# Kernel optimization log

Measured on AMD Instinct MI355X. Metric: run time of the kernel, lower is better.

The kernel has to match this reference:

```python
import jax, jax.numpy as jnp
import numpy as np

EPS = 1e-6      # fast_transformers LinearAttention eps
LN_EPS = 1e-5   # torch LayerNorm default
L_LAYERS = 4
N_HEADS = 16
D_MODEL = 1024
D_FF = 4096


def _layernorm(x, g, b):
    mu = jnp.mean(x, axis=-1, keepdims=True)
    var = jnp.mean(jnp.square(x - mu), axis=-1, keepdims=True)
    return (x - mu) * jax.lax.rsqrt(var + LN_EPS) * g + b


def _layer(x, fmask, Wq, bq, Wk, bk, Wv, bv, Wo, bo, W1, b1, W2, b2, g1, be1, g2, be2):
    N, S, D = x.shape
    H = N_HEADS
    d = D // H
    q = (x @ Wq.T + bq).reshape(N, S, H, d)
    k = (x @ Wk.T + bk).reshape(N, S, H, d)
    v = (x @ Wv.T + bv).reshape(N, S, H, d)
    # feature map: elu(x) + 1
    Q = jax.nn.elu(q) + 1.0
    K = (jax.nn.elu(k) + 1.0) * fmask[:, :, None, None]
    # non-causal linear attention
    KV = jnp.einsum('nshd,nshm->nhmd', K, v)                       # [N,H,d,d]
    Z = 1.0 / (jnp.einsum('nlhd,nhd->nlh', Q, K.sum(axis=1)) + EPS)
    attn = jnp.einsum('nlhd,nhmd,nlh->nlhm', Q, KV, Z).reshape(N, S, D)
    x = x + (attn @ Wo.T + bo)
    y = x = _layernorm(x, g1, be1)
    y = jax.nn.gelu(y @ W1.T + b1, approximate=False) @ W2.T + b2
    return _layernorm(x + y, g2, be2)


def setup_inputs() -> dict:
    key = jax.random.key(0)
    ks = jax.random.split(key, 12)
    N, S, D, F = 4, 4096, D_MODEL, D_FF
    L = L_LAYERS
    s = 0.02
    inp = {
        'src': jax.random.normal(ks[0], (N, S, D), dtype=jnp.float32),
        'src_key_padding_mask': jnp.zeros((N, S), dtype=bool),
        'Wq': jax.random.normal(ks[1], (L, D, D), dtype=jnp.float32) * s,
        'bq': jnp.zeros((L, D), dtype=jnp.float32),
        'Wk': jax.random.normal(ks[2], (L, D, D), dtype=jnp.float32) * s,
        'bk': jnp.zeros((L, D), dtype=jnp.float32),
        'Wv': jax.random.normal(ks[3], (L, D, D), dtype=jnp.float32) * s,
        'bv': jnp.zeros((L, D), dtype=jnp.float32),
        'Wo': jax.random.normal(ks[4], (L, D, D), dtype=jnp.float32) * s,
        'bo': jnp.zeros((L, D), dtype=jnp.float32),
        'W1': jax.random.normal(ks[5], (L, F, D), dtype=jnp.float32) * s,
        'b1': jnp.zeros((L, F), dtype=jnp.float32),
        'W2': jax.random.normal(ks[6], (L, D, F), dtype=jnp.float32) * s,
        'b2': jnp.zeros((L, D), dtype=jnp.float32),
        'g1': jnp.ones((L, D), dtype=jnp.float32),
        'be1': jnp.zeros((L, D), dtype=jnp.float32),
        'g2': jnp.ones((L, D), dtype=jnp.float32),
        'be2': jnp.zeros((L, D), dtype=jnp.float32),
    }
    return inp


def reference(src, src_key_padding_mask, Wq, bq, Wk, bk, Wv, bv, Wo, bo,
              W1, b1, W2, b2, g1, be1, g2, be2):
    N, S, D = src.shape
    # LengthMask: valid positions are the first (S - num_paddings) tokens
    actual_len = S - src_key_padding_mask.sum(axis=1)              # [N]
    fmask = (jnp.arange(S)[None, :] < actual_len[:, None]).astype(src.dtype)
    x = src
    for i in range(L_LAYERS):
        x = _layer(x, fmask, Wq[i], bq[i], Wk[i], bk[i], Wv[i], bv[i],
                   Wo[i], bo[i], W1[i], b1[i], W2[i], b2[i],
                   g1[i], be1[i], g2[i], be2[i])
    return x
```

## Files before the change

kernel.cpp:

```cpp
#include <hip/hip_runtime.h>
#include <cstdint>

typedef unsigned short ushort_t;
typedef short v8s __attribute__((ext_vector_type(8)));
typedef float v4f __attribute__((ext_vector_type(4)));
typedef unsigned short v4u __attribute__((ext_vector_type(4)));

#define DMODEL 1024
#define DFF 4096
#define SEQ 4096
#define NBATCH 4
#define NHEAD 16
#define HDIM 64
#define NLAYER 4
#define MTOK (NBATCH*SEQ)

#define EPI_QKV 0
#define EPI_RES 3
#define EPI_GELU 4

__device__ __forceinline__ float bf2f(ushort_t u) {
    unsigned v = ((unsigned)u) << 16; float f; __builtin_memcpy(&f, &v, 4); return f;
}
__device__ __forceinline__ ushort_t f2bf(float f) {
    unsigned u; __builtin_memcpy(&u, &f, 4);
    u = (u + 0x7fffu + ((u >> 16) & 1u)) >> 16;
    return (ushort_t)u;
}

__device__ __forceinline__ float gelu_f(float x) {
    const float y = x * 0.70710678118f;
    const float ay = fabsf(y);
    const float t = __builtin_amdgcn_rcpf(1.f + 0.3275911f * ay);
    const float p = t * (0.254829592f + t * (-0.284496736f + t * (1.421413741f +
                    t * (-1.453152027f + t * 1.061405429f))));
    const float e = __expf(-y * y);
    float er = 1.f - p * e;
    er = (y < 0.f) ? -er : er;
    return 0.5f * x * (1.f + er);
}

__global__ __launch_bounds__(256) void cvt_bf16(const float* __restrict__ in,
                                                ushort_t* __restrict__ out, int n) {
    int i = (blockIdx.x * 256 + threadIdx.x) * 4;
    if (i >= n) return;
    float4 v = *(const float4*)(in + i);
    v4u o;
    o[0] = f2bf(v.x); o[1] = f2bf(v.y); o[2] = f2bf(v.z); o[3] = f2bf(v.w);
    *(v4u*)(out + i) = o;
}

__global__ __launch_bounds__(256) void cvt_qkv(const float* __restrict__ Wq,
                                               const float* __restrict__ Wk,
                                               const float* __restrict__ Wv,
                                               ushort_t* __restrict__ out) {
    const size_t DD = (size_t)DMODEL * DMODEL;
    size_t i = ((size_t)blockIdx.x * 256 + threadIdx.x) * 4;
    int l = (int)(i / DD);
    size_t r = i % DD;
    const float* srcs[3] = { Wq + l * DD + r, Wk + l * DD + r, Wv + l * DD + r };
    #pragma unroll
    for (int s = 0; s < 3; s++) {
        float4 v = *(const float4*)srcs[s];
        v4u o;
        o[0] = f2bf(v.x); o[1] = f2bf(v.y); o[2] = f2bf(v.z); o[3] = f2bf(v.w);
        *(v4u*)(out + ((size_t)l * 3 + s) * DD + r) = o;
    }
}

__global__ __launch_bounds__(256) void lens_kernel(const unsigned char* __restrict__ mask,
                                                   int* __restrict__ lens) {
    int lane = threadIdx.x & 63, w = threadIdx.x >> 6;
    int cnt = 0;
    for (int i = lane; i < SEQ; i += 64) cnt += (mask[w * SEQ + i] != 0) ? 1 : 0;
    #pragma unroll
    for (int off = 32; off; off >>= 1) cnt += __shfl_down(cnt, off);
    if (lane == 0) lens[w] = SEQ - cnt;
}

template <int EPI>
__global__ __launch_bounds__(256, 2) void gemm_bt(
    const ushort_t* __restrict__ A, const ushort_t* __restrict__ B,
    const float* __restrict__ bias, const float* __restrict__ bias2,
    const float* __restrict__ bias3, const float* res,
    const int* __restrict__ lens,
    ushort_t* __restrict__ outB, ushort_t* __restrict__ outB2,
    ushort_t* __restrict__ outB3, float* outF,
    int M, int N, int K)
{
    __shared__ __align__(16) ushort_t As[2][128 * 64];
    __shared__ __align__(16) ushort_t Bs[2][128 * 64];

    const int tid = threadIdx.x;
    const int lane = tid & 63;
    const int wave = tid >> 6;
    const int nb = N >> 7;
    const int xcd = blockIdx.x & 7;
    const int q = blockIdx.x >> 3;
    const int bm = (q / nb) * 8 + xcd;
    const int bn = q % nb;
    const int wm = (wave >> 1) * 64;
    const int wn = (wave & 1) * 64;
    const int lr = lane & 15;
    const int lq = lane >> 4;

    v4f acc[4][4];
    #pragma unroll
    for (int i = 0; i < 4; i++)
        #pragma unroll
        for (int j = 0; j < 4; j++) acc[i][j] = (v4f)0.f;

    const int srow = tid >> 3;
    const int schunk = (tid & 7) ^ (srow & 7);
    const ushort_t* Ag = A + (size_t)(bm * 128 + srow) * K + schunk * 8;
    const ushort_t* Bg = B + (size_t)(bn * 128 + srow) * K + schunk * 8;
    const size_t rstep = (size_t)32 * K;
    const int sdst = tid * 8;

    int a_off[2][4], b_off[2][4];
    #pragma unroll
    for (int h = 0; h < 2; h++)
        #pragma unroll
        for (int i = 0; i < 4; i++) {
            const int ra = wm + i * 16 + lr;
            a_off[h][i] = ra * 64 + (((h * 4 + lq) ^ (ra & 7)) * 8);
            const int rb = wn + i * 16 + lr;
            b_off[h][i] = rb * 64 + (((h * 4 + lq) ^ (rb & 7)) * 8);
        }

    v8s ra[4], rb[4];
    #pragma unroll
    for (int i = 0; i < 4; i++) ra[i] = *(const v8s*)(Ag + i * rstep);
    #pragma unroll
    for (int i = 0; i < 4; i++) rb[i] = *(const v8s*)(Bg + i * rstep);

    const int iters = K >> 6;
    int p = 0;
    for (int t = 0; t < iters; ++t) {
        #pragma unroll
        for (int i = 0; i < 4; i++) *(v8s*)&As[p][sdst + i * 2048] = ra[i];
        #pragma unroll
        for (int i = 0; i < 4; i++) *(v8s*)&Bs[p][sdst + i * 2048] = rb[i];
        if (t + 1 < iters) {
            const int k0 = (t + 1) << 6;
            #pragma unroll
            for (int i = 0; i < 4; i++) ra[i] = *(const v8s*)(Ag + i * rstep + k0);
            #pragma unroll
            for (int i = 0; i < 4; i++) rb[i] = *(const v8s*)(Bg + i * rstep + k0);
        }
        __syncthreads();
        #pragma unroll
        for (int h = 0; h < 2; h++) {
            v8s af[4], bfr[4];
            #pragma unroll
            for (int i = 0; i < 4; i++) af[i] = *(const v8s*)&As[p][a_off[h][i]];
            #pragma unroll
            for (int j = 0; j < 4; j++) bfr[j] = *(const v8s*)&Bs[p][b_off[h][j]];
            #pragma unroll
            for (int i = 0; i < 4; i++)
                #pragma unroll
                for (int j = 0; j < 4; j++)
                    acc[i][j] = __builtin_amdgcn_mfma_f32_16x16x32_bf16(af[i], bfr[j], acc[i][j], 0, 0, 0);
        }
        p ^= 1;
    }

    const int row0 = bm * 128 + wm + lq * 4;
    const int col0 = bn * 128 + wn + lr;

    const int seg = bn >> 3;
    ushort_t* qkv_out = (EPI == EPI_QKV)
        ? (seg == 0 ? outB : (seg == 1 ? outB2 : outB3)) : outB;
    const float* qkv_bias = (EPI == EPI_QKV)
        ? (seg == 0 ? bias : (seg == 1 ? bias2 : bias3)) : bias;
    const int blen = (EPI == EPI_QKV) ? lens[bm >> 5] : 0;

    #pragma unroll
    for (int i = 0; i < 4; i++) {
        #pragma unroll
        for (int j = 0; j < 4; j++) {
            const int gn = col0 + j * 16;
            const float bsv = (EPI == EPI_QKV) ? qkv_bias[gn & 1023] : bias[gn];
            #pragma unroll
            for (int r = 0; r < 4; r++) {
                const int gm = row0 + i * 16 + r;
                float v = acc[i][j][r] + bsv;
                if (EPI == EPI_QKV) {
                    const size_t oi = (size_t)gm * DMODEL + (gn & 1023);
                    if (seg == 2) {
                        qkv_out[oi] = f2bf(v);
                    } else {
                        float e = v > 0.f ? v + 1.f : __expf(v);
                        if (seg == 1 && (gm & 4095) >= blen) e = 0.f;
                        qkv_out[oi] = f2bf(e);
                    }
                } else if (EPI == EPI_RES) {
                    const size_t oi = (size_t)gm * N + gn;
                    outF[oi] = v + res[oi];
                } else {
                    const size_t oi = (size_t)gm * N + gn;
                    outB[oi] = f2bf(gelu_f(v));
                }
            }
        }
    }
}

__global__ __launch_bounds__(256) void ksum_kernel(const ushort_t* __restrict__ K,
                                                   float* __restrict__ out) {
    const int blk = blockIdx.x;
    const int n = blk >> 4, cg = blk & 15;
    const int tx = threadIdx.x & 63, ty = threadIdx.x >> 6;
    const int col = cg * 64 + tx;
    const ushort_t* p = K + ((size_t)n * SEQ + ty * 1024) * DMODEL + col;
    float a = 0.f;
    for (int s = 0; s < 1024; s++) a += bf2f(p[(size_t)s * DMODEL]);
    __shared__ float red[4][64];
    red[ty][tx] = a;
    __syncthreads();
    if (ty == 0) out[n * DMODEL + col] = red[0][tx] + red[1][tx] + red[2][tx] + red[3][tx];
}

__global__ __launch_bounds__(256) void kv_part(const ushort_t* __restrict__ K,
                                               const ushort_t* __restrict__ V,
                                               float* __restrict__ part) {
    const int chunk = blockIdx.x, nh = blockIdx.y;
    const int n = nh >> 4, h = nh & 15;
    const int tid = threadIdx.x;
    const int tm = tid >> 4, td = tid & 15;
    __shared__ float Ks[16][68];
    __shared__ float Vs[16][68];
    float acc[4][4] = {};
    const int s0 = chunk * 512;
    for (int sb = 0; sb < 512; sb += 16) {
        __syncthreads();
        for (int idx = tid; idx < 1024; idx += 256) {
            const int r = idx >> 6, c = idx & 63;
            const size_t gpos = ((size_t)(n * SEQ + s0 + sb + r)) * DMODEL + h * HDIM + c;
            Ks[r][c] = bf2f(K[gpos]);
            Vs[r][c] = bf2f(V[gpos]);
        }
        __syncthreads();
        #pragma unroll
        for (int s = 0; s < 16; s++) {
            float kv[4], vv[4];
            #pragma unroll
            for (int j = 0; j < 4; j++) kv[j] = Ks[s][td * 4 + j];
            #pragma unroll
            for (int i = 0; i < 4; i++) vv[i] = Vs[s][tm * 4 + i];
            #pragma unroll
            for (int i = 0; i < 4; i++)
                #pragma unroll
                for (int j = 0; j < 4; j++)
                    acc[i][j] += vv[i] * kv[j];
        }
    }
    float* o = part + ((size_t)chunk * 64 + nh) * 4096;
    #pragma unroll
    for (int i = 0; i < 4; i++)
        #pragma unroll
        for (int j = 0; j < 4; j++)
            o[(tm * 4 + i) * 64 + td * 4 + j] = acc[i][j];
}

__global__ __launch_bounds__(256) void kv_reduce(const float* __restrict__ part,
                                                 float* __restrict__ KV) {
    const int gid = blockIdx.x * 256 + threadIdx.x;
    float a = 0.f;
    #pragma unroll
    for (int c = 0; c < 8; c++) a += part[(size_t)c * (64 * 4096) + gid];
    KV[gid] = a;
}

__global__ __launch_bounds__(256) void attn_kernel(const ushort_t* __restrict__ Q,
                                                   const float* __restrict__ KV,
                                                   const float* __restrict__ Ksum,
                                                   ushort_t* __restrict__ out) {
    const int bx = blockIdx.x, nh = blockIdx.y;
    const int n = nh >> 4, h = nh & 15;
    const int tid = threadIdx.x;
    const int ty = tid >> 4, tx = tid & 15;
    __shared__ float KVs[64][65];
    __shared__ float Qs[64][65];
    __shared__ float Zs[64];
    const int t0 = n * SEQ + bx * 64;
    for (int idx = tid; idx < 4096; idx += 256) {
        const int r = idx >> 6, c = idx & 63;
        KVs[r][c] = KV[(size_t)nh * 4096 + idx];
        Qs[r][c] = bf2f(Q[((size_t)(t0 + r)) * DMODEL + h * HDIM + c]);
    }
    __syncthreads();
    if (tid < 64) {
        const float* ks = Ksum + n * DMODEL + h * HDIM;
        float a = 0.f;
        #pragma unroll
        for (int d = 0; d < 64; d++) a += Qs[tid][d] * ks[d];
        Zs[tid] = 1.f / (a + 1e-6f);
    }
    __syncthreads();
    float acc[4][4] = {};
    for (int d = 0; d < 64; d++) {
        float qv[4], kv[4];
        #pragma unroll
        for (int i = 0; i < 4; i++) qv[i] = Qs[ty * 4 + i][d];
        #pragma unroll
        for (int j = 0; j < 4; j++) kv[j] = KVs[tx * 4 + j][d];
        #pragma unroll
        for (int i = 0; i < 4; i++)
            #pragma unroll
            for (int j = 0; j < 4; j++)
                acc[i][j] += qv[i] * kv[j];
    }
    #pragma unroll
    for (int i = 0; i < 4; i++) {
        const int r = ty * 4 + i;
        const float z = Zs[r];
        v4u o;
        #pragma unroll
        for (int j = 0; j < 4; j++) o[j] = f2bf(acc[i][j] * z);
        *(v4u*)&out[((size_t)(t0 + r)) * DMODEL + h * HDIM + tx * 4] = o;
    }
}

__global__ __launch_bounds__(256) void ln_kernel(const float* in, float* outF,
                                                 ushort_t* outB,
                                                 const float* __restrict__ g,
                                                 const float* __restrict__ b) {
    const int row = blockIdx.x;
    const int tid = threadIdx.x;
    const float4 v = ((const float4*)(in + (size_t)row * DMODEL))[tid];
    float s = v.x + v.y + v.z + v.w;
    float ss = v.x * v.x + v.y * v.y + v.z * v.z + v.w * v.w;
    #pragma unroll
    for (int off = 32; off; off >>= 1) {
        s += __shfl_down(s, off);
        ss += __shfl_down(ss, off);
    }
    __shared__ float red[8];
    const int lane = tid & 63, w = tid >> 6;
    if (lane == 0) { red[w * 2] = s; red[w * 2 + 1] = ss; }
    __syncthreads();
    s = red[0] + red[2] + red[4] + red[6];
    ss = red[1] + red[3] + red[5] + red[7];
    const float mu = s * (1.f / DMODEL);
    const float var = ss * (1.f / DMODEL) - mu * mu;
    const float rs = rsqrtf(var + 1e-5f);
    const float4 gg = ((const float4*)g)[tid];
    const float4 bb = ((const float4*)b)[tid];
    float4 o;
    o.x = (v.x - mu) * rs * gg.x + bb.x;
    o.y = (v.y - mu) * rs * gg.y + bb.y;
    o.z = (v.z - mu) * rs * gg.z + bb.z;
    o.w = (v.w - mu) * rs * gg.w + bb.w;
    ((float4*)(outF + (size_t)row * DMODEL))[tid] = o;
    if (outB) {
        v4u ob;
        ob[0] = f2bf(o.x); ob[1] = f2bf(o.y); ob[2] = f2bf(o.z); ob[3] = f2bf(o.w);
        *(v4u*)(outB + (size_t)row * DMODEL + tid * 4) = ob;
    }
}

extern "C" void kernel_launch(void* const* d_in, const int* in_sizes, int n_in,
                              void* d_out, int out_size, void* d_ws, size_t ws_size,
                              hipStream_t stream) {
    const float* src = (const float*)d_in[0];
    const unsigned char* mask = (const unsigned char*)d_in[1];
    const float* Wq = (const float*)d_in[2];
    const float* bq = (const float*)d_in[3];
    const float* Wk = (const float*)d_in[4];
    const float* bk = (const float*)d_in[5];
    const float* Wv = (const float*)d_in[6];
    const float* bv = (const float*)d_in[7];
    const float* Wo = (const float*)d_in[8];
    const float* bo = (const float*)d_in[9];
    const float* W1 = (const float*)d_in[10];
    const float* b1 = (const float*)d_in[11];
    const float* W2 = (const float*)d_in[12];
    const float* b2 = (const float*)d_in[13];
    const float* g1 = (const float*)d_in[14];
    const float* be1 = (const float*)d_in[15];
    const float* g2 = (const float*)d_in[16];
    const float* be2 = (const float*)d_in[17];

    float* xout = (float*)d_out;

    char* ws = (char*)d_ws;
    size_t off = 0;
    auto alloc = [&](size_t bytes) -> void* {
        void* p = (void*)(ws + off);
        off += (bytes + 255) & ~(size_t)255;
        return p;
    };
    const size_t DD = (size_t)DMODEL * DMODEL;
    const size_t FD = (size_t)DFF * DMODEL;
    const size_t MD = (size_t)MTOK * DMODEL;

    ushort_t* wqkv_bf = (ushort_t*)alloc(NLAYER * 3 * DD * 2);
    ushort_t* wo_bf = (ushort_t*)alloc(NLAYER * DD * 2);
    ushort_t* w1r = (ushort_t*)alloc(FD * 2);
    ushort_t* w2r = (ushort_t*)alloc(FD * 2);
    ushort_t* xbf = (ushort_t*)alloc(MD * 2);
    ushort_t* Qb = (ushort_t*)alloc(MD * 2);
    ushort_t* Kb = (ushort_t*)alloc(MD * 2);
    ushort_t* Vb = (ushort_t*)alloc(MD * 2);
    (void)alloc(MD * 2);
    ushort_t* hb = Qb;
    float* Ksum = (float*)alloc((size_t)NBATCH * DMODEL * 4);
    float* KVp = (float*)alloc((size_t)8 * 64 * 4096 * 4);
    float* KVb = (float*)alloc((size_t)64 * 4096 * 4);
    int* lens = (int*)alloc(256);
    if (off > ws_size) return;

    cvt_qkv<<<dim3((unsigned)((NLAYER * DD) / 1024)), dim3(256), 0, stream>>>(Wq, Wk, Wv, wqkv_bf);
    cvt_bf16<<<dim3((unsigned)((NLAYER * DD) / 1024)), dim3(256), 0, stream>>>(Wo, wo_bf, (int)(NLAYER * DD));
    lens_kernel<<<dim3(1), dim3(256), 0, stream>>>(mask, lens);
    cvt_bf16<<<dim3((unsigned)(MD / 1024)), dim3(256), 0, stream>>>(src, xbf, (int)MD);

    const dim3 blk(256);
    const dim3 gQKV((MTOK / 128) * (3 * DMODEL / 128));
    const dim3 gD((MTOK / 128) * (DMODEL / 128));
    const dim3 gF((MTOK / 128) * (DFF / 128));

    for (int l = 0; l < NLAYER; l++) {
        const ushort_t* wqkvl = wqkv_bf + (size_t)l * 3 * DD;
        const ushort_t* wol = wo_bf + l * DD;
        const float* bql = bq + l * DMODEL;
        const float* bkl = bk + l * DMODEL;
        const float* bvl = bv + l * DMODEL;
        const float* bol = bo + l * DMODEL;
        const float* b1l = b1 + l * DFF;
        const float* b2l = b2 + l * DMODEL;
        const float* g1l = g1 + l * DMODEL;
        const float* be1l = be1 + l * DMODEL;
        const float* g2l = g2 + l * DMODEL;
        const float* be2l = be2 + l * DMODEL;
        const float* resx = (l == 0) ? src : xout;

        gemm_bt<EPI_QKV><<<gQKV, blk, 0, stream>>>(xbf, wqkvl, bql, bkl, bvl,
            nullptr, lens, Qb, Kb, Vb, nullptr, MTOK, 3 * DMODEL, DMODEL);

        ksum_kernel<<<dim3(64), blk, 0, stream>>>(Kb, Ksum);
        kv_part<<<dim3(8, 64), blk, 0, stream>>>(Kb, Vb, KVp);
        kv_reduce<<<dim3(64 * 4096 / 256), blk, 0, stream>>>(KVp, KVb);
        attn_kernel<<<dim3(64, 64), blk, 0, stream>>>(Qb, KVb, Ksum, Kb);

        gemm_bt<EPI_RES><<<gD, blk, 0, stream>>>(Kb, wol, bol, nullptr, nullptr,
            resx, lens, nullptr, nullptr, nullptr, xout, MTOK, DMODEL, DMODEL);
        ln_kernel<<<dim3(MTOK), blk, 0, stream>>>(xout, xout, xbf, g1l, be1l);

        cvt_bf16<<<dim3((unsigned)(FD / 1024)), blk, 0, stream>>>(W1 + l * FD, w1r, (int)FD);
        gemm_bt<EPI_GELU><<<gF, blk, 0, stream>>>(xbf, w1r, b1l, nullptr, nullptr,
            nullptr, lens, hb, nullptr, nullptr, nullptr, MTOK, DFF, DMODEL);
        cvt_bf16<<<dim3((unsigned)(FD / 1024)), blk, 0, stream>>>(W2 + l * FD, w2r, (int)FD);
        gemm_bt<EPI_RES><<<gD, blk, 0, stream>>>(hb, w2r, b2l, nullptr, nullptr,
            xout, lens, nullptr, nullptr, nullptr, xout, MTOK, DMODEL, DFF);
        ln_kernel<<<dim3(MTOK), blk, 0, stream>>>(xout, xout, (l == NLAYER - 1) ? nullptr : xbf, g2l, be2l);
    }
}
```

Before: 3.278 ms.

## Rewrite GEMM with 256x256 tiles, direct global-to-LDS loads and phased MFMA

The bf16 GEMM moves from 128x128 tiles with 256 threads to 256x256 tiles with 512 threads (8 waves, each computing 128x64). Tiles are loaded straight into LDS with global_load_lds, two tiles ahead, and explicit vmcnt waits and barriers replace register staging. The MFMA loop is split into four phases with priority boosts so LDS reads interleave with compute. The aim is more reuse per byte loaded and better overlap of memory with MFMA. The cost is 128KB of LDS per block, which limits occupancy, and grids that are 4x smaller, which may underfill the CUs.

```diff
diff --git a/kernel.cpp b/kernel.cpp
--- a/kernel.cpp
+++ b/kernel.cpp
@@ -40,6 +40,12 @@
     return 0.5f * x * (1.f + er);
 }
 
+__device__ __forceinline__ void gload16(const ushort_t* g, ushort_t* l) {
+    __builtin_amdgcn_global_load_lds(
+        (__attribute__((address_space(1))) unsigned int*)g,
+        (__attribute__((address_space(3))) unsigned int*)l, 16, 0, 0);
+}
+
 __global__ __launch_bounds__(256) void cvt_bf16(const float* __restrict__ in,
                                                 ushort_t* __restrict__ out, int n) {
     int i = (blockIdx.x * 256 + threadIdx.x) * 4;
@@ -78,8 +84,13 @@
     if (lane == 0) lens[w] = SEQ - cnt;
 }
 
+#define BAR()    asm volatile("s_barrier" ::: "memory")
+#define WAITL0() asm volatile("s_waitcnt lgkmcnt(0)" ::: "memory")
+#define WAITV8() asm volatile("s_waitcnt vmcnt(8)" ::: "memory")
+#define WAITV0() asm volatile("s_waitcnt vmcnt(0)" ::: "memory")
+
 template <int EPI>
-__global__ __launch_bounds__(256, 2) void gemm_bt(
+__global__ __launch_bounds__(512, 2) void gemm_bt(
     const ushort_t* __restrict__ A, const ushort_t* __restrict__ B,
     const float* __restrict__ bias, const float* __restrict__ bias2,
     const float* __restrict__ bias3, const float* res,
@@ -88,95 +99,122 @@
     ushort_t* __restrict__ outB3, float* outF,
     int M, int N, int K)
 {
-    __shared__ __align__(16) ushort_t As[2][128 * 64];
-    __shared__ __align__(16) ushort_t Bs[2][128 * 64];
+    __shared__ __align__(16) ushort_t As[2][256 * 64];
+    __shared__ __align__(16) ushort_t Bs[2][256 * 64];
 
     const int tid = threadIdx.x;
     const int lane = tid & 63;
-    const int wave = tid >> 6;
-    const int nb = N >> 7;
+    const int w = tid >> 6;
+    const int wm = w >> 2;
+    const int wn = w & 3;
+    const int nb = N >> 8;
     const int xcd = blockIdx.x & 7;
     const int q = blockIdx.x >> 3;
     const int bm = (q / nb) * 8 + xcd;
     const int bn = q % nb;
-    const int wm = (wave >> 1) * 64;
-    const int wn = (wave & 1) * 64;
     const int lr = lane & 15;
     const int lq = lane >> 4;
 
-    v4f acc[4][4];
-    #pragma unroll
-    for (int i = 0; i < 4; i++)
+    v4f acc[8][4];
+    #pragma unroll
+    for (int i = 0; i < 8; i++)
         #pragma unroll
         for (int j = 0; j < 4; j++) acc[i][j] = (v4f)0.f;
 
-    const int srow = tid >> 3;
-    const int schunk = (tid & 7) ^ (srow & 7);
-    const ushort_t* Ag = A + (size_t)(bm * 128 + srow) * K + schunk * 8;
-    const ushort_t* Bg = B + (size_t)(bn * 128 + srow) * K + schunk * 8;
-    const size_t rstep = (size_t)32 * K;
-    const int sdst = tid * 8;
-
-    int a_off[2][4], b_off[2][4];
-    #pragma unroll
-    for (int h = 0; h < 2; h++)
-        #pragma unroll
-        for (int i = 0; i < 4; i++) {
-            const int ra = wm + i * 16 + lr;
-            a_off[h][i] = ra * 64 + (((h * 4 + lq) ^ (ra & 7)) * 8);
-            const int rb = wn + i * 16 + lr;
-            b_off[h][i] = rb * 64 + (((h * 4 + lq) ^ (rb & 7)) * 8);
-        }
-
-    v8s ra[4], rb[4];
-    #pragma unroll
-    for (int i = 0; i < 4; i++) ra[i] = *(const v8s*)(Ag + i * rstep);
-    #pragma unroll
-    for (int i = 0; i < 4; i++) rb[i] = *(const v8s*)(Bg + i * rstep);
-
-    const int iters = K >> 6;
-    int p = 0;
-    for (int t = 0; t < iters; ++t) {
-        #pragma unroll
-        for (int i = 0; i < 4; i++) *(v8s*)&As[p][sdst + i * 2048] = ra[i];
-        #pragma unroll
-        for (int i = 0; i < 4; i++) *(v8s*)&Bs[p][sdst + i * 2048] = rb[i];
-        if (t + 1 < iters) {
-            const int k0 = (t + 1) << 6;
-            #pragma unroll
-            for (int i = 0; i < 4; i++) ra[i] = *(const v8s*)(Ag + i * rstep + k0);
-            #pragma unroll
-            for (int i = 0; i < 4; i++) rb[i] = *(const v8s*)(Bg + i * rstep + k0);
-        }
-        __syncthreads();
-        #pragma unroll
-        for (int h = 0; h < 2; h++) {
-            v8s af[4], bfr[4];
-            #pragma unroll
-            for (int i = 0; i < 4; i++) af[i] = *(const v8s*)&As[p][a_off[h][i]];
-            #pragma unroll
-            for (int j = 0; j < 4; j++) bfr[j] = *(const v8s*)&Bs[p][b_off[h][j]];
-            #pragma unroll
-            for (int i = 0; i < 4; i++)
-                #pragma unroll
-                for (int j = 0; j < 4; j++)
-                    acc[i][j] = __builtin_amdgcn_mfma_f32_16x16x32_bf16(af[i], bfr[j], acc[i][j], 0, 0, 0);
-        }
-        p ^= 1;
-    }
-
-    const int row0 = bm * 128 + wm + lq * 4;
-    const int col0 = bn * 128 + wn + lr;
-
-    const int seg = bn >> 3;
+    const int srow = lane >> 3;
+    const int schunk = (lane & 7) ^ srow;
+    const ushort_t* Ag = A + (size_t)(bm * 256 + srow) * K + schunk * 8;
+    const ushort_t* Bg = B + (size_t)(bn * 256 + srow) * K + schunk * 8;
+
+    int aoff[2], boff[2];
+    #pragma unroll
+    for (int kh = 0; kh < 2; kh++) {
+        aoff[kh] = (wm * 128 + lr) * 64 + (((kh * 4 + lq) ^ (lr & 7)) * 8);
+        boff[kh] = (wn * 64 + lr) * 64 + (((kh * 4 + lq) ^ (lr & 7)) * 8);
+    }
+
+    const int KT = K >> 6;
+
+#define ISSUE_TILE(T_, P_) do { \
+    const size_t kk_ = (size_t)(T_) << 6; \
+    _Pragma("unroll") \
+    for (int i_ = 0; i_ < 4; i_++) { \
+        const int c_ = (w << 2) + i_; \
+        gload16(Ag + (size_t)c_ * 8 * K + kk_, &As[P_][c_ << 9]); \
+        gload16(Bg + (size_t)c_ * 8 * K + kk_, &Bs[P_][c_ << 9]); \
+    } \
+} while (0)
+
+#define READ_B(P_) do { \
+    _Pragma("unroll") \
+    for (int j_ = 0; j_ < 4; j_++) \
+        _Pragma("unroll") \
+        for (int kh_ = 0; kh_ < 2; kh_++) \
+            bfr[j_][kh_] = *(const v8s*)&Bs[P_][boff[kh_] + j_ * 1024]; \
+} while (0)
+
+#define READ_A(P_, QQ) do { \
+    _Pragma("unroll") \
+    for (int i_ = 0; i_ < 2; i_++) \
+        _Pragma("unroll") \
+        for (int kh_ = 0; kh_ < 2; kh_++) \
+            af[i_][kh_] = *(const v8s*)&As[P_][aoff[kh_] + (QQ) * 2048 + i_ * 1024]; \
+} while (0)
+
+#define MFMA_PHASE(QQ) do { \
+    BAR(); WAITL0(); \
+    __builtin_amdgcn_s_setprio(1); \
+    _Pragma("unroll") \
+    for (int i_ = 0; i_ < 2; i_++) \
+        _Pragma("unroll") \
+        for (int j_ = 0; j_ < 4; j_++) \
+            _Pragma("unroll") \
+            for (int kh_ = 0; kh_ < 2; kh_++) \
+                acc[(QQ) * 2 + i_][j_] = __builtin_amdgcn_mfma_f32_16x16x32_bf16( \
+                    af[i_][kh_], bfr[j_][kh_], acc[(QQ) * 2 + i_][j_], 0, 0, 0); \
+    __builtin_amdgcn_s_setprio(0); \
+} while (0)
+
+#define TILE_BODY(T_, P_) do { \
+    v8s af[2][2]; v8s bfr[4][2]; \
+    READ_B(P_); READ_A(P_, 0); \
+    MFMA_PHASE(0); BAR(); \
+    READ_A(P_, 1); MFMA_PHASE(1); BAR(); \
+    READ_A(P_, 2); MFMA_PHASE(2); BAR(); \
+    READ_A(P_, 3); MFMA_PHASE(3); \
+    if ((T_) + 2 < KT) { ISSUE_TILE((T_) + 2, P_); WAITV8(); } \
+    else if ((T_) + 1 < KT) { WAITV0(); } \
+    BAR(); \
+} while (0)
+
+    ISSUE_TILE(0, 0);
+    ISSUE_TILE(1, 1);
+    WAITV8();
+    BAR();
+
+    for (int t = 0; t < KT; t += 2) {
+        TILE_BODY(t, 0);
+        TILE_BODY(t + 1, 1);
+    }
+
+#undef TILE_BODY
+#undef MFMA_PHASE
+#undef READ_A
+#undef READ_B
+#undef ISSUE_TILE
+
+    const int row0 = bm * 256 + wm * 128 + lq * 4;
+    const int col0 = bn * 256 + wn * 64 + lr;
+
+    const int seg = (EPI == EPI_QKV) ? (bn >> 2) : 0;
     ushort_t* qkv_out = (EPI == EPI_QKV)
         ? (seg == 0 ? outB : (seg == 1 ? outB2 : outB3)) : outB;
     const float* qkv_bias = (EPI == EPI_QKV)
         ? (seg == 0 ? bias : (seg == 1 ? bias2 : bias3)) : bias;
-    const int blen = (EPI == EPI_QKV) ? lens[bm >> 5] : 0;
-
-    #pragma unroll
-    for (int i = 0; i < 4; i++) {
+    const int blen = (EPI == EPI_QKV) ? lens[bm >> 4] : 0;
+
+    #pragma unroll
+    for (int i = 0; i < 8; i++) {
         #pragma unroll
         for (int j = 0; j < 4; j++) {
             const int gn = col0 + j * 16;
@@ -417,9 +455,10 @@
     cvt_bf16<<<dim3((unsigned)(MD / 1024)), dim3(256), 0, stream>>>(src, xbf, (int)MD);
 
     const dim3 blk(256);
-    const dim3 gQKV((MTOK / 128) * (3 * DMODEL / 128));
-    const dim3 gD((MTOK / 128) * (DMODEL / 128));
-    const dim3 gF((MTOK / 128) * (DFF / 128));
+    const dim3 blkG(512);
+    const dim3 gQKV((MTOK / 256) * (3 * DMODEL / 256));
+    const dim3 gD((MTOK / 256) * (DMODEL / 256));
+    const dim3 gF((MTOK / 256) * (DFF / 256));
 
     for (int l = 0; l < NLAYER; l++) {
         const ushort_t* wqkvl = wqkv_bf + (size_t)l * 3 * DD;
@@ -436,7 +475,7 @@
         const float* be2l = be2 + l * DMODEL;
         const float* resx = (l == 0) ? src : xout;
 
-        gemm_bt<EPI_QKV><<<gQKV, blk, 0, stream>>>(xbf, wqkvl, bql, bkl, bvl,
+        gemm_bt<EPI_QKV><<<gQKV, blkG, 0, stream>>>(xbf, wqkvl, bql, bkl, bvl,
             nullptr, lens, Qb, Kb, Vb, nullptr, MTOK, 3 * DMODEL, DMODEL);
 
         ksum_kernel<<<dim3(64), blk, 0, stream>>>(Kb, Ksum);
@@ -444,15 +483,15 @@
         kv_reduce<<<dim3(64 * 4096 / 256), blk, 0, stream>>>(KVp, KVb);
         attn_kernel<<<dim3(64, 64), blk, 0, stream>>>(Qb, KVb, Ksum, Kb);
 
-        gemm_bt<EPI_RES><<<gD, blk, 0, stream>>>(Kb, wol, bol, nullptr, nullptr,
+        gemm_bt<EPI_RES><<<gD, blkG, 0, stream>>>(Kb, wol, bol, nullptr, nullptr,
             resx, lens, nullptr, nullptr, nullptr, xout, MTOK, DMODEL, DMODEL);
         ln_kernel<<<dim3(MTOK), blk, 0, stream>>>(xout, xout, xbf, g1l, be1l);
 
         cvt_bf16<<<dim3((unsigned)(FD / 1024)), blk, 0, stream>>>(W1 + l * FD, w1r, (int)FD);
-        gemm_bt<EPI_GELU><<<gF, blk, 0, stream>>>(xbf, w1r, b1l, nullptr, nullptr,
+        gemm_bt<EPI_GELU><<<gF, blkG, 0, stream>>>(xbf, w1r, b1l, nullptr, nullptr,
             nullptr, lens, hb, nullptr, nullptr, nullptr, MTOK, DFF, DMODEL);
         cvt_bf16<<<dim3((unsigned)(FD / 1024)), blk, 0, stream>>>(W2 + l * FD, w2r, (int)FD);
-        gemm_bt<EPI_RES><<<gD, blk, 0, stream>>>(hb, w2r, b2l, nullptr, nullptr,
+        gemm_bt<EPI_RES><<<gD, blkG, 0, stream>>>(hb, w2r, b2l, nullptr, nullptr,
             xout, lens, nullptr, nullptr, nullptr, xout, MTOK, DMODEL, DFF);
         ln_kernel<<<dim3(MTOK), blk, 0, stream>>>(xout, xout, (l == NLAYER - 1) ? nullptr : xbf, g2l, be2l);
     }
```

Result: slower. 3.384 ms (+3.2%).

## Load GEMM tiles directly into LDS and raise occupancy to four blocks

Applied to the files above, without the earlier changes.

The GEMM main loop no longer stages tiles through registers into a double-buffered LDS area. It now uses global_load_lds to copy each 16-byte chunk straight into a single LDS buffer, with a barrier before and after each load. Freeing the staging registers and halving LDS per block lets launch bounds request four resident blocks per CU. Overlap of loads with compute now comes from other resident blocks rather than in-block prefetch, so the extra barrier per iteration may expose latency.

```diff
diff --git a/kernel.cpp b/kernel.cpp
--- a/kernel.cpp
+++ b/kernel.cpp
@@ -40,6 +40,12 @@
     return 0.5f * x * (1.f + er);
 }
 
+__device__ __forceinline__ void gload16(const ushort_t* g, ushort_t* l) {
+    __builtin_amdgcn_global_load_lds(
+        (__attribute__((address_space(1))) unsigned int*)g,
+        (__attribute__((address_space(3))) unsigned int*)l, 16, 0, 0);
+}
+
 __global__ __launch_bounds__(256) void cvt_bf16(const float* __restrict__ in,
                                                 ushort_t* __restrict__ out, int n) {
     int i = (blockIdx.x * 256 + threadIdx.x) * 4;
@@ -79,7 +85,7 @@
 }
 
 template <int EPI>
-__global__ __launch_bounds__(256, 2) void gemm_bt(
+__global__ __launch_bounds__(256, 4) void gemm_bt(
     const ushort_t* __restrict__ A, const ushort_t* __restrict__ B,
     const float* __restrict__ bias, const float* __restrict__ bias2,
     const float* __restrict__ bias3, const float* res,
@@ -88,8 +94,8 @@
     ushort_t* __restrict__ outB3, float* outF,
     int M, int N, int K)
 {
-    __shared__ __align__(16) ushort_t As[2][128 * 64];
-    __shared__ __align__(16) ushort_t Bs[2][128 * 64];
+    __shared__ __align__(16) ushort_t As[128 * 64];
+    __shared__ __align__(16) ushort_t Bs[128 * 64];
 
     const int tid = threadIdx.x;
     const int lane = tid & 63;
@@ -114,7 +120,6 @@
     const int schunk = (tid & 7) ^ (srow & 7);
     const ushort_t* Ag = A + (size_t)(bm * 128 + srow) * K + schunk * 8;
     const ushort_t* Bg = B + (size_t)(bn * 128 + srow) * K + schunk * 8;
-    const size_t rstep = (size_t)32 * K;
     const int sdst = tid * 8;
 
     int a_off[2][4], b_off[2][4];
@@ -128,47 +133,36 @@
             b_off[h][i] = rb * 64 + (((h * 4 + lq) ^ (rb & 7)) * 8);
         }
 
-    v8s ra[4], rb[4];
-    #pragma unroll
-    for (int i = 0; i < 4; i++) ra[i] = *(const v8s*)(Ag + i * rstep);
-    #pragma unroll
-    for (int i = 0; i < 4; i++) rb[i] = *(const v8s*)(Bg + i * rstep);
-
     const int iters = K >> 6;
-    int p = 0;
     for (int t = 0; t < iters; ++t) {
-        #pragma unroll
-        for (int i = 0; i < 4; i++) *(v8s*)&As[p][sdst + i * 2048] = ra[i];
-        #pragma unroll
-        for (int i = 0; i < 4; i++) *(v8s*)&Bs[p][sdst + i * 2048] = rb[i];
-        if (t + 1 < iters) {
-            const int k0 = (t + 1) << 6;
-            #pragma unroll
-            for (int i = 0; i < 4; i++) ra[i] = *(const v8s*)(Ag + i * rstep + k0);
-            #pragma unroll
-            for (int i = 0; i < 4; i++) rb[i] = *(const v8s*)(Bg + i * rstep + k0);
-        }
+        __syncthreads();
+        const size_t kk = (size_t)t * 64;
+        #pragma unroll
+        for (int i = 0; i < 4; i++)
+            gload16(Ag + (size_t)i * 32 * K + kk, &As[sdst + i * 2048]);
+        #pragma unroll
+        for (int i = 0; i < 4; i++)
+            gload16(Bg + (size_t)i * 32 * K + kk, &Bs[sdst + i * 2048]);
         __syncthreads();
         #pragma unroll
         for (int h = 0; h < 2; h++) {
             v8s af[4], bfr[4];
             #pragma unroll
-            for (int i = 0; i < 4; i++) af[i] = *(const v8s*)&As[p][a_off[h][i]];
-            #pragma unroll
-            for (int j = 0; j < 4; j++) bfr[j] = *(const v8s*)&Bs[p][b_off[h][j]];
+            for (int i = 0; i < 4; i++) af[i] = *(const v8s*)&As[a_off[h][i]];
+            #pragma unroll
+            for (int j = 0; j < 4; j++) bfr[j] = *(const v8s*)&Bs[b_off[h][j]];
             #pragma unroll
             for (int i = 0; i < 4; i++)
                 #pragma unroll
                 for (int j = 0; j < 4; j++)
                     acc[i][j] = __builtin_amdgcn_mfma_f32_16x16x32_bf16(af[i], bfr[j], acc[i][j], 0, 0, 0);
         }
-        p ^= 1;
     }
 
     const int row0 = bm * 128 + wm + lq * 4;
     const int col0 = bn * 128 + wn + lr;
 
-    const int seg = bn >> 3;
+    const int seg = (EPI == EPI_QKV) ? (bn >> 3) : 0;
     ushort_t* qkv_out = (EPI == EPI_QKV)
         ? (seg == 0 ? outB : (seg == 1 ? outB2 : outB3)) : outB;
     const float* qkv_bias = (EPI == EPI_QKV)
```

Measured after the change: 3.024 ms. 7.7% less time.
